# Kernel tuning notes

Measured on AMD Instinct MI355X. Metric: run time of the kernel, lower is better.

## Reference

```python
import jax, jax.numpy as jnp
import numpy as np

EPS = 1e-5

def _bn_relu_over_batch(x, gamma, beta):
    # x: [..., B, F] where batch axis is -2; per-step training-mode BatchNorm1d
    mu = x.mean(axis=-2, keepdims=True)
    var = ((x - mu) ** 2).mean(axis=-2, keepdims=True)  # biased var (torch BN)
    xn = (x - mu) * jax.lax.rsqrt(var + EPS)
    return jax.nn.relu(xn * gamma + beta)

def setup_inputs() -> dict:
    key = jax.random.key(0)
    ks = jax.random.split(key, 8)
    B, T, D_in, E, C, D_out = 8192, 128, 2, 128, 128, 5
    s = 0.1
    return {
        "inputs": jax.random.normal(ks[0], (B, T, D_in), jnp.float32),
        "W_emb": jax.random.normal(ks[1], (E, D_in), jnp.float32) * s,
        "b_emb": jnp.zeros((E,), jnp.float32),
        "g_emb": jnp.ones((E,), jnp.float32),
        "be_emb": jnp.zeros((E,), jnp.float32),
        "W_ih": jax.random.normal(ks[2], (4 * C, E), jnp.float32) * s,
        "W_hh": jax.random.normal(ks[3], (4 * C, C), jnp.float32) * s,
        "b_ih": jnp.zeros((4 * C,), jnp.float32),
        "b_hh": jnp.zeros((4 * C,), jnp.float32),
        "W_out": jax.random.normal(ks[4], (D_out, C), jnp.float32) * s,
        "b_out": jnp.zeros((D_out,), jnp.float32),
        "g_out": jnp.ones((D_out,), jnp.float32),
        "be_out": jnp.zeros((D_out,), jnp.float32),
    }

def reference(inputs, W_emb, b_emb, g_emb, be_emb, W_ih, W_hh, b_ih, b_hh,
              W_out, b_out, g_out, be_out):
    B, T, _ = inputs.shape
    C = W_hh.shape[1]
    # Input embedding: Linear + per-step BatchNorm (batch stats) + ReLU, vectorized over T
    x = jnp.einsum('btd,ed->bte', inputs, W_emb) + b_emb      # [B,T,E]
    x = jnp.transpose(x, (1, 0, 2))                           # [T,B,E]
    x = _bn_relu_over_batch(x, g_emb, be_emb)                 # BN over batch per step

    def step(carry, xt):
        h, c = carry
        gates = xt @ W_ih.T + b_ih + h @ W_hh.T + b_hh        # [B,4C]
        i, f, g, o = jnp.split(gates, 4, axis=-1)             # torch LSTMCell order
        i = jax.nn.sigmoid(i); f = jax.nn.sigmoid(f)
        g = jnp.tanh(g); o = jax.nn.sigmoid(o)
        c = f * c + i * g
        h = o * jnp.tanh(c)
        return (h, c), h

    h0 = jnp.zeros((B, C), inputs.dtype)
    _, h_all = jax.lax.scan(step, (h0, h0), x)                # [T,B,C]

    # Output embedding: Linear + per-step BatchNorm + ReLU
    y = jnp.einsum('tbc,oc->tbo', h_all, W_out) + b_out       # [T,B,5]
    y = _bn_relu_over_batch(y, g_out, be_out)
    return jnp.transpose(y, (1, 0, 2))                        # [B,T,5]
```

## Files before the change

kernel.cpp:

```cpp
#include <hip/hip_runtime.h>

typedef __attribute__((ext_vector_type(8))) short short8;
typedef __attribute__((ext_vector_type(4))) float floatx4;
typedef __attribute__((ext_vector_type(4))) unsigned int uint4v;

#define B_TOT 8192
#define T_STEPS 128
#define E_DIM 128
#define C_DIM 128
#define D_OUT 5
#define BN_EPS 1e-5f

#define LOG2E 1.4426950408889634f
#define TWO_LOG2E 2.8853900817779268f

#define WS_WCAT   0u
#define WS_WOUT   (WS_WCAT + 262144u)
#define WS_A0     (WS_WOUT + 4096u)
#define WS_A1     (WS_A0 + 65536u)
#define WS_CC     (WS_A1 + 65536u)
#define WS_STATS  (WS_CC + 65536u)
#define WS_PART   (WS_STATS + 5120u)
#define WS_Y      (WS_PART + 20480u)

__device__ __forceinline__ float bf2f(unsigned short h){
  return __uint_as_float(((unsigned int)h) << 16);
}
__device__ __forceinline__ unsigned short f2b(float v){
  unsigned int u = __float_as_uint(v);
  u += 0x7FFFu + ((u >> 16) & 1u);
  return (unsigned short)(u >> 16);
}
__device__ __forceinline__ unsigned cvt_pk_bf16(float lo, float hi){
  unsigned r;
  asm("v_cvt_pk_bf16_f32 %0, %1, %2" : "=v"(r) : "v"(lo), "v"(hi));
  return r;
}
__device__ __forceinline__ float ldf(const void* p, int i, int bf){
  return bf ? bf2f(((const unsigned short*)p)[i]) : ((const float*)p)[i];
}
__device__ __forceinline__ int sniff_bf(const void* ones){
  return *(const unsigned int*)ones == 0x3F803F80u;
}

__global__ void k_prep_mom(const void* W_ih, const void* W_hh, const void* W_out,
                           unsigned short* wcat, unsigned short* wout,
                           const void* x, float* part, const void* ones){
  const int bf = sniff_bf(ones);
  const int tid = threadIdx.x;
  if (blockIdx.x < 260){
    int i = blockIdx.x * 512 + tid;
    if (i < 512*256){
      int n = i >> 8, k = i & 255;
      float v = (k < 128) ? ldf(W_ih, n*128 + k, bf) : ldf(W_hh, n*128 + (k-128), bf);
      float sc = ((n >> 7) == 2) ? TWO_LOG2E : -LOG2E;
      wcat[i] = f2b(v * sc);
    } else {
      int j = i - 512*256;
      int n = j >> 7, k = j & 127;
      float v = (n < D_OUT) ? ldf(W_out, n*128 + k, bf) : 0.0f;
      wout[j] = f2b(v);
    }
    return;
  }
  const int mb  = blockIdx.x - 260;
  const int wdw = (mb >> 3) * 8;
  const int rg  = mb & 7;
  const int wv = tid >> 6, lane = tid & 63;
  __shared__ float red[8][16][3];

  if (!bf){
    const float* xp = (const float*)x;
    const int row_b = tid >> 4, j = tid & 15;
    float a0=0, a1=0, a2=0;
    for (int c = 0; c < 32; ++c){
      int row = rg*1024 + c*32 + row_b;
      float v = xp[row*256 + wdw*2 + j];
      float p = __shfl_xor(v, 1, 64);
      if ((j & 1) == 0){ a0 += v; a1 += v*v; a2 += v*p; }
      else             { a0 += v; a1 += v*v; }
    }
    a0 += __shfl_down(a0,32,64); a0 += __shfl_down(a0,16,64);
    a1 += __shfl_down(a1,32,64); a1 += __shfl_down(a1,16,64);
    a2 += __shfl_down(a2,32,64); a2 += __shfl_down(a2,16,64);
    if (lane < 16){ red[wv][lane][0]=a0; red[wv][lane][1]=a1; red[wv][lane][2]=a2; }
  } else {
    const unsigned int* xp = (const unsigned int*)x;
    const int row_b = tid >> 3, j = tid & 7;
    float s0=0,s1=0,s00=0,s11=0,s01=0;
    for (int c = 0; c < 16; ++c){
      int row = rg*1024 + c*64 + row_b;
      unsigned int u = xp[row*128 + wdw + j];
      float xv0 = bf2f((unsigned short)(u & 0xFFFFu));
      float xv1 = bf2f((unsigned short)(u >> 16));
      s0+=xv0; s1+=xv1; s00+=xv0*xv0; s11+=xv1*xv1; s01+=xv0*xv1;
    }
    s0 += __shfl_down(s0,32,64); s0 += __shfl_down(s0,16,64); s0 += __shfl_down(s0,8,64);
    s1 += __shfl_down(s1,32,64); s1 += __shfl_down(s1,16,64); s1 += __shfl_down(s1,8,64);
    s00+= __shfl_down(s00,32,64);s00+= __shfl_down(s00,16,64);s00+= __shfl_down(s00,8,64);
    s11+= __shfl_down(s11,32,64);s11+= __shfl_down(s11,16,64);s11+= __shfl_down(s11,8,64);
    s01+= __shfl_down(s01,32,64);s01+= __shfl_down(s01,16,64);s01+= __shfl_down(s01,8,64);
    if (lane < 8){
      red[wv][lane][0]=s0;  red[wv][lane][1]=s00; red[wv][lane][2]=s01;
      red[wv][8+lane][0]=s1; red[wv][8+lane][1]=s11;
    }
  }
  __syncthreads();
  if (tid < 8){
    int tl = tid;
    float S0=0,S1=0,S00=0,S11=0,S01=0;
    for (int w8 = 0; w8 < 8; ++w8){
      if (!bf){
        S0 += red[w8][2*tl][0];   S00 += red[w8][2*tl][1];   S01 += red[w8][2*tl][2];
        S1 += red[w8][2*tl+1][0]; S11 += red[w8][2*tl+1][1];
      } else {
        S0 += red[w8][tl][0];     S00 += red[w8][tl][1];     S01 += red[w8][tl][2];
        S1 += red[w8][8+tl][0];   S11 += red[w8][8+tl][1];
      }
    }
    float* dst = part + rg*640 + (wdw + tl)*5;
    dst[0]=S0; dst[1]=S1; dst[2]=S00; dst[3]=S11; dst[4]=S01;
  }
}

__global__ void k_coef(const float* part, const void* W_emb, const void* g_emb, const void* be_emb,
                       float* A0, float* A1, float* Cc){
  const int bf = sniff_bf(g_emb);
  int i = blockIdx.x*256 + threadIdx.x;
  int t = i >> 7, e = i & 127;
  float S0=0,S1=0,S00=0,S11=0,S01=0;
  for (int rg = 0; rg < 8; ++rg){
    const float* p = part + rg*640 + t*5;
    S0+=p[0]; S1+=p[1]; S00+=p[2]; S11+=p[3]; S01+=p[4];
  }
  const float inv = 1.0f / (float)B_TOT;
  float mu0 = S0*inv, mu1 = S1*inv;
  float v00 = S00*inv - mu0*mu0, v11 = S11*inv - mu1*mu1, c01 = S01*inv - mu0*mu1;
  float w0 = ldf(W_emb, e*2, bf), w1 = ldf(W_emb, e*2+1, bf);
  float g  = ldf(g_emb, e, bf),  be = ldf(be_emb, e, bf);
  float var = w0*w0*v00 + 2.0f*w0*w1*c01 + w1*w1*v11;
  float rs = rsqrtf(var + BN_EPS);
  float a0 = g*rs*w0, a1 = g*rs*w1;
  A0[i] = a0; A1[i] = a1;
  Cc[i] = be - (a0*mu0 + a1*mu1);
}

__global__ __launch_bounds__(512, 2)
void k_lstm(const void* x, const void* b_ih, const void* b_hh, const void* ones,
            const unsigned short* __restrict__ wcat, const unsigned short* __restrict__ wout,
            const float* __restrict__ A0, const float* __restrict__ A1, const float* __restrict__ Cc,
            float* __restrict__ y_ws){
  const int bf = sniff_bf(ones);
  const int tid = threadIdx.x;
  const int wid = tid >> 6, lane = tid & 63;
  const int q = lane >> 4, s = lane & 15;
  const int row0 = blockIdx.x * 32;

  __shared__ unsigned short xh[2][32][264];

  {
    short8 z;
#pragma unroll
    for (int j = 0; j < 8; ++j) z[j] = 0;
    unsigned short* base = &xh[0][0][0];
    for (int i = tid*8; i < 2*32*264; i += 512*8)
      *(short8*)(base + i) = z;
  }

  short8 bfr[4][8];
#pragma unroll
  for (int gq = 0; gq < 4; ++gq)
#pragma unroll
    for (int ks = 0; ks < 8; ++ks)
      bfr[gq][ks] = *(const short8*)(wcat + ((wid + 8*gq)*16 + s)*256 + ks*32 + q*8);

  short8 wf[4];
#pragma unroll
  for (int ks = 0; ks < 4; ++ks)
    wf[ks] = *(const short8*)(wout + s*128 + ks*32 + q*8);

  const int ch = 16*wid + s;
  floatx4 binit[4];
#pragma unroll
  for (int gq = 0; gq < 4; ++gq){
    float braw = ldf(b_ih, gq*128 + ch, bf) + ldf(b_hh, gq*128 + ch, bf);
    float b = braw * ((gq == 2) ? TWO_LOG2E : -LOG2E);
    binit[gq] = (floatx4){b, b, b, b};
  }

  float c_st[2][4] = {{0,0,0,0},{0,0,0,0}};

  const int r_loc = tid >> 4;
  const int e0 = (tid & 15) * 8;

  auto compute_xe = [&](int tt, int buf){
    float x0, x1;
    int xbase = ((row0 + r_loc)*T_STEPS + tt)*2;
    if (bf){
      unsigned u = ((const unsigned int*)x)[xbase >> 1];
      x0 = __uint_as_float(u << 16);
      x1 = __uint_as_float(u & 0xFFFF0000u);
    } else { const float* xp = (const float*)x; x0 = xp[xbase]; x1 = xp[xbase+1]; }
    floatx4 a0a = *(const floatx4*)(A0 + tt*E_DIM + e0);
    floatx4 a0b = *(const floatx4*)(A0 + tt*E_DIM + e0 + 4);
    floatx4 a1a = *(const floatx4*)(A1 + tt*E_DIM + e0);
    floatx4 a1b = *(const floatx4*)(A1 + tt*E_DIM + e0 + 4);
    floatx4 cca = *(const floatx4*)(Cc + tt*E_DIM + e0);
    floatx4 ccb = *(const floatx4*)(Cc + tt*E_DIM + e0 + 4);
    float v[8];
#pragma unroll
    for (int j = 0; j < 4; ++j){
      v[j]   = fmaxf(fmaf(a0a[j], x0, fmaf(a1a[j], x1, cca[j])), 0.0f);
      v[4+j] = fmaxf(fmaf(a0b[j], x0, fmaf(a1b[j], x1, ccb[j])), 0.0f);
    }
    unsigned w0 = cvt_pk_bf16(v[0], v[1]);
    unsigned w1 = cvt_pk_bf16(v[2], v[3]);
    unsigned w2 = cvt_pk_bf16(v[4], v[5]);
    unsigned w3 = cvt_pk_bf16(v[6], v[7]);
    *(uint4v*)&xh[buf][r_loc][e0] = (uint4v){w0, w1, w2, w3};
  };

  auto cell = [&](const floatx4* acc, float* cs, int mt, int nb){
    float hv[4];
#pragma unroll
    for (int r = 0; r < 4; ++r){
      float ea = __builtin_amdgcn_exp2f(acc[0][r]);
      float eb = __builtin_amdgcn_exp2f(acc[1][r]);
      float ec = __builtin_amdgcn_exp2f(acc[2][r]);
      float ed = __builtin_amdgcn_exp2f(acc[3][r]);
      float Aa = 1.0f + ea, Bb = 1.0f + eb, Ca = 1.0f + ec;
      float t1 = Aa * Ca;
      float r1 = __builtin_amdgcn_rcpf(t1 * Bb);
      float cn = fmaf(t1 * r1, cs[r], (Bb * r1) * (ec - 1.0f));
      cs[r] = cn;
      float E  = __builtin_amdgcn_exp2f(fminf(cn * TWO_LOG2E, 80.0f));
      float r2 = __builtin_amdgcn_rcpf((1.0f + ed) * (E + 1.0f));
      hv[r] = (E - 1.0f) * r2;
    }
    unsigned wlo = cvt_pk_bf16(hv[0], hv[1]);
    unsigned whi = cvt_pk_bf16(hv[2], hv[3]);
    const int rowb = 16*mt + q*4;
    xh[nb][rowb    ][128 + ch] = (unsigned short)(wlo);
    xh[nb][rowb + 1][128 + ch] = (unsigned short)(wlo >> 16);
    xh[nb][rowb + 2][128 + ch] = (unsigned short)(whi);
    xh[nb][rowb + 3][128 + ch] = (unsigned short)(whi >> 16);
  };

  auto step = [&](int t, int cb, int nb){
    if (wid < 2 && t > 0){
      floatx4 ya = {0,0,0,0};
#pragma unroll
      for (int ks = 0; ks < 4; ++ks){
        short8 a = *(const short8*)&xh[cb][s + 16*wid][128 + ks*32 + q*8];
        ya = __builtin_amdgcn_mfma_f32_16x16x32_bf16(a, wf[ks], ya, 0, 0, 0);
      }
      if (s < D_OUT){
#pragma unroll
        for (int r = 0; r < 4; ++r){
          int row = row0 + 16*wid + q*4 + r;
          y_ws[((t-1)*B_TOT + row)*D_OUT + s] = ya[r];
        }
      }
    }

    floatx4 acc0[4], acc1[4];

    {
      short8 a0 = *(const short8*)&xh[cb][s][q*8];
#pragma unroll
      for (int gq = 0; gq < 4; ++gq)
        acc0[gq] = __builtin_amdgcn_mfma_f32_16x16x32_bf16(a0, bfr[gq][0], binit[gq], 0, 0, 0);
    }
#pragma unroll
    for (int ks = 1; ks < 8; ++ks){
      short8 a0 = *(const short8*)&xh[cb][s][ks*32 + q*8];
#pragma unroll
      for (int gq = 0; gq < 4; ++gq)
        acc0[gq] = __builtin_amdgcn_mfma_f32_16x16x32_bf16(a0, bfr[gq][ks], acc0[gq], 0, 0, 0);
    }
    {
      short8 a1 = *(const short8*)&xh[cb][s + 16][q*8];
#pragma unroll
      for (int gq = 0; gq < 4; ++gq)
        acc1[gq] = __builtin_amdgcn_mfma_f32_16x16x32_bf16(a1, bfr[gq][0], binit[gq], 0, 0, 0);
    }
#pragma unroll
    for (int ks = 1; ks < 8; ++ks){
      short8 a1 = *(const short8*)&xh[cb][s + 16][ks*32 + q*8];
#pragma unroll
      for (int gq = 0; gq < 4; ++gq)
        acc1[gq] = __builtin_amdgcn_mfma_f32_16x16x32_bf16(a1, bfr[gq][ks], acc1[gq], 0, 0, 0);
    }

    if (t < T_STEPS-1) compute_xe(t+1, nb);

    cell(acc0, c_st[0], 0, nb);
    cell(acc1, c_st[1], 1, nb);

    __syncthreads();
  };

  __syncthreads();
  compute_xe(0, 0);
  __syncthreads();

  for (int tb = 0; tb < T_STEPS; tb += 2){
    step(tb,     0, 1);
    step(tb + 1, 1, 0);
  }

  if (wid < 2){
    floatx4 ya = {0,0,0,0};
#pragma unroll
    for (int ks = 0; ks < 4; ++ks){
      short8 a = *(const short8*)&xh[0][s + 16*wid][128 + ks*32 + q*8];
      ya = __builtin_amdgcn_mfma_f32_16x16x32_bf16(a, wf[ks], ya, 0, 0, 0);
    }
    if (s < D_OUT){
#pragma unroll
      for (int r = 0; r < 4; ++r){
        int row = row0 + 16*wid + q*4 + r;
        y_ws[((T_STEPS-1)*B_TOT + row)*D_OUT + s] = ya[r];
      }
    }
  }
  asm volatile("s_waitcnt vmcnt(0)" ::: "memory");
}

__global__ void k_outstats(const float* __restrict__ y_ws, const void* g_out, const void* be_out,
                           float* stats, const void* ones){
  const int bf = sniff_bf(ones);
  const int t = blockIdx.x, tid = threadIdx.x;
  __shared__ float acc2[5][2];
  if (tid < 10) ((float*)acc2)[tid] = 0.0f;
  __syncthreads();
  float s[5] = {0,0,0,0,0}, ss[5] = {0,0,0,0,0};
  const floatx4* base = (const floatx4*)(y_ws + (size_t)t * 40960);
#pragma unroll 5
  for (int it = 0; it < 40; ++it){
    floatx4 v = base[it*256 + tid];
#pragma unroll
    for (int j = 0; j < 4; ++j){
      int p = (4*it + j) % 5;
      s[p] += v[j]; ss[p] += v[j]*v[j];
    }
  }
  int ob = (4*tid) % 5;
#pragma unroll
  for (int p = 0; p < 5; ++p){
    int o = ob + p; if (o >= 5) o -= 5;
    atomicAdd(&acc2[o][0], s[p]);
    atomicAdd(&acc2[o][1], ss[p]);
  }
  __syncthreads();
  if (tid < 5){
    float S = acc2[tid][0], SS = acc2[tid][1];
    const float inv = 1.0f / (float)B_TOT;
    float mu = S*inv, var = SS*inv - mu*mu;
    float g = ldf(g_out, tid, bf), be = ldf(be_out, tid, bf);
    float sc = g * rsqrtf(var + BN_EPS);
    stats[(t*5+tid)*2]   = sc;
    stats[(t*5+tid)*2+1] = be - sc*mu;
  }
}

__global__ void k_apply(const float* __restrict__ y_ws, const float* __restrict__ stats,
                        void* out, const void* ones){
  const int bf = sniff_bf(ones);
  __shared__ float tile[128*85];
  const int b0 = blockIdx.x * 16;
  const int tid = threadIdx.x;
  for (int i = tid; i < 10240; i += 256){
    int t = i / 80, j = i - t*80;
    tile[t*85 + j] = y_ws[((size_t)t*B_TOT + b0)*D_OUT + j];
  }
  __syncthreads();
  for (int i = tid; i < 10240; i += 256){
    int b = i / 640, r = i - b*640;
    int t = r / 5, o = r - t*5;
    float v = tile[t*85 + b*5 + o];
    v = fmaxf(fmaf(v, stats[r*2], stats[r*2+1]), 0.0f);
    int oi = b0*640 + i;
    if (bf) ((unsigned short*)out)[oi] = f2b(v);
    else    ((float*)out)[oi] = v;
  }
}

extern "C" void kernel_launch(void* const* d_in, const int* in_sizes, int n_in,
                              void* d_out, int out_size, void* d_ws, size_t ws_size,
                              hipStream_t stream){
  const void* x      = d_in[0];
  const void* W_emb  = d_in[1];
  const void* g_emb  = d_in[3];
  const void* be_emb = d_in[4];
  const void* W_ih   = d_in[5];
  const void* W_hh   = d_in[6];
  const void* b_ih   = d_in[7];
  const void* b_hh   = d_in[8];
  const void* W_out  = d_in[9];
  const void* g_out  = d_in[11];
  const void* be_out = d_in[12];

  char* ws = (char*)d_ws;
  unsigned short* wcat = (unsigned short*)(ws + WS_WCAT);
  unsigned short* wout = (unsigned short*)(ws + WS_WOUT);
  float* A0    = (float*)(ws + WS_A0);
  float* A1    = (float*)(ws + WS_A1);
  float* Cc    = (float*)(ws + WS_CC);
  float* stats = (float*)(ws + WS_STATS);
  float* part  = (float*)(ws + WS_PART);
  float* y_ws  = (float*)(ws + WS_Y);

  k_prep_mom<<<dim3(388),  dim3(512), 0, stream>>>(W_ih, W_hh, W_out, wcat, wout, x, part, g_emb);
  k_coef    <<<dim3(64),   dim3(256), 0, stream>>>(part, W_emb, g_emb, be_emb, A0, A1, Cc);
  k_lstm    <<<dim3(256),  dim3(512), 0, stream>>>(x, b_ih, b_hh, g_emb, wcat, wout, A0, A1, Cc, y_ws);
  k_outstats<<<dim3(128),  dim3(256), 0, stream>>>(y_ws, g_out, be_out, stats, g_emb);
  k_apply   <<<dim3(512),  dim3(256), 0, stream>>>(y_ws, stats, d_out, g_emb);
}
```

Measured before the change: 375.3 us.

## Fuse output BN statistics into LSTM kernel via atomics, drop stats kernel

The LSTM kernel now reduces each step's output-projection sums and sums of squares with wave shuffles and global atomics, so the separate output-statistics kernel and its full pass over y are removed. The y workspace layout changes to [t][o][b], which allows vectorized float4 stores and coalesced reads in the apply kernel. The apply kernel now computes scale and bias from the accumulated sums itself. The cost is extra atomics and shuffle work inside the latency-critical recurrent loop, plus a buffer that must be zeroed by the prep kernel.

```diff
diff --git a/kernel.cpp b/kernel.cpp
--- a/kernel.cpp
+++ b/kernel.cpp
@@ -19,8 +19,8 @@
 #define WS_A0     (WS_WOUT + 4096u)
 #define WS_A1     (WS_A0 + 65536u)
 #define WS_CC     (WS_A1 + 65536u)
-#define WS_STATS  (WS_CC + 65536u)
-#define WS_PART   (WS_STATS + 5120u)
+#define WS_YSUM   (WS_CC + 65536u)
+#define WS_PART   (WS_YSUM + 5120u)
 #define WS_Y      (WS_PART + 20480u)
 
 __device__ __forceinline__ float bf2f(unsigned short h){
@@ -45,9 +45,12 @@
 
 __global__ void k_prep_mom(const void* W_ih, const void* W_hh, const void* W_out,
                            unsigned short* wcat, unsigned short* wout,
-                           const void* x, float* part, const void* ones){
+                           const void* x, float* part, float* ysum, const void* ones){
   const int bf = sniff_bf(ones);
   const int tid = threadIdx.x;
+  if (blockIdx.x == 0){
+    for (int i2 = tid; i2 < 1280; i2 += 512) ysum[i2] = 0.0f;
+  }
   if (blockIdx.x < 260){
     int i = blockIdx.x * 512 + tid;
     if (i < 512*256){
@@ -149,7 +152,7 @@
 void k_lstm(const void* x, const void* b_ih, const void* b_hh, const void* ones,
             const unsigned short* __restrict__ wcat, const unsigned short* __restrict__ wout,
             const float* __restrict__ A0, const float* __restrict__ A1, const float* __restrict__ Cc,
-            float* __restrict__ y_ws){
+            float* __restrict__ y_ws, float* __restrict__ ysum){
   const int bf = sniff_bf(ones);
   const int tid = threadIdx.x;
   const int wid = tid >> 6, lane = tid & 63;
@@ -246,22 +249,27 @@
     xh[nb][rowb + 3][128 + ch] = (unsigned short)(whi >> 16);
   };
 
+  auto do_y = [&](int tt, int hb){
+    floatx4 ya = {0,0,0,0};
+#pragma unroll
+    for (int ks = 0; ks < 4; ++ks){
+      short8 a = *(const short8*)&xh[hb][s + 16*wid][128 + ks*32 + q*8];
+      ya = __builtin_amdgcn_mfma_f32_16x16x32_bf16(a, wf[ks], ya, 0, 0, 0);
+    }
+    if (s < D_OUT)
+      *(floatx4*)(y_ws + ((size_t)tt*D_OUT + s)*B_TOT + row0 + 16*wid + 4*q) = ya;
+    float ps  = ya[0] + ya[1] + ya[2] + ya[3];
+    float pss = ya[0]*ya[0] + ya[1]*ya[1] + ya[2]*ya[2] + ya[3]*ya[3];
+    ps  += __shfl_down(ps, 32, 64); ps  += __shfl_down(ps, 16, 64);
+    pss += __shfl_down(pss, 32, 64); pss += __shfl_down(pss, 16, 64);
+    if (lane < D_OUT){
+      atomicAdd(&ysum[(tt*D_OUT + lane)*2],     ps);
+      atomicAdd(&ysum[(tt*D_OUT + lane)*2 + 1], pss);
+    }
+  };
+
   auto step = [&](int t, int cb, int nb){
-    if (wid < 2 && t > 0){
-      floatx4 ya = {0,0,0,0};
-#pragma unroll
-      for (int ks = 0; ks < 4; ++ks){
-        short8 a = *(const short8*)&xh[cb][s + 16*wid][128 + ks*32 + q*8];
-        ya = __builtin_amdgcn_mfma_f32_16x16x32_bf16(a, wf[ks], ya, 0, 0, 0);
-      }
-      if (s < D_OUT){
-#pragma unroll
-        for (int r = 0; r < 4; ++r){
-          int row = row0 + 16*wid + q*4 + r;
-          y_ws[((t-1)*B_TOT + row)*D_OUT + s] = ya[r];
-        }
-      }
-    }
+    if (wid < 2 && t > 0) do_y(t-1, cb);
 
     floatx4 acc0[4], acc1[4];
 
@@ -309,77 +317,36 @@
     step(tb + 1, 1, 0);
   }
 
-  if (wid < 2){
-    floatx4 ya = {0,0,0,0};
-#pragma unroll
-    for (int ks = 0; ks < 4; ++ks){
-      short8 a = *(const short8*)&xh[0][s + 16*wid][128 + ks*32 + q*8];
-      ya = __builtin_amdgcn_mfma_f32_16x16x32_bf16(a, wf[ks], ya, 0, 0, 0);
-    }
-    if (s < D_OUT){
-#pragma unroll
-      for (int r = 0; r < 4; ++r){
-        int row = row0 + 16*wid + q*4 + r;
-        y_ws[((T_STEPS-1)*B_TOT + row)*D_OUT + s] = ya[r];
-      }
-    }
-  }
+  if (wid < 2) do_y(T_STEPS-1, 0);
+
   asm volatile("s_waitcnt vmcnt(0)" ::: "memory");
 }
 
-__global__ void k_outstats(const float* __restrict__ y_ws, const void* g_out, const void* be_out,
-                           float* stats, const void* ones){
+__global__ void k_apply(const float* __restrict__ y_ws, const float* __restrict__ ysum,
+                        void* out, const void* g_out, const void* be_out, const void* ones){
   const int bf = sniff_bf(ones);
-  const int t = blockIdx.x, tid = threadIdx.x;
-  __shared__ float acc2[5][2];
-  if (tid < 10) ((float*)acc2)[tid] = 0.0f;
-  __syncthreads();
-  float s[5] = {0,0,0,0,0}, ss[5] = {0,0,0,0,0};
-  const floatx4* base = (const floatx4*)(y_ws + (size_t)t * 40960);
-#pragma unroll 5
-  for (int it = 0; it < 40; ++it){
-    floatx4 v = base[it*256 + tid];
-#pragma unroll
-    for (int j = 0; j < 4; ++j){
-      int p = (4*it + j) % 5;
-      s[p] += v[j]; ss[p] += v[j]*v[j];
-    }
-  }
-  int ob = (4*tid) % 5;
-#pragma unroll
-  for (int p = 0; p < 5; ++p){
-    int o = ob + p; if (o >= 5) o -= 5;
-    atomicAdd(&acc2[o][0], s[p]);
-    atomicAdd(&acc2[o][1], ss[p]);
-  }
-  __syncthreads();
-  if (tid < 5){
-    float S = acc2[tid][0], SS = acc2[tid][1];
+  __shared__ float sc_l[640], bi_l[640];
+  __shared__ float tile[10240];
+  const int b0 = blockIdx.x * 16;
+  const int tid = threadIdx.x;
+  for (int i = tid; i < 640; i += 256){
+    float S = ysum[i*2], SS = ysum[i*2+1];
     const float inv = 1.0f / (float)B_TOT;
     float mu = S*inv, var = SS*inv - mu*mu;
-    float g = ldf(g_out, tid, bf), be = ldf(be_out, tid, bf);
+    int o = i % 5;
+    float g = ldf(g_out, o, bf), be = ldf(be_out, o, bf);
     float sc = g * rsqrtf(var + BN_EPS);
-    stats[(t*5+tid)*2]   = sc;
-    stats[(t*5+tid)*2+1] = be - sc*mu;
-  }
-}
-
-__global__ void k_apply(const float* __restrict__ y_ws, const float* __restrict__ stats,
-                        void* out, const void* ones){
-  const int bf = sniff_bf(ones);
-  __shared__ float tile[128*85];
-  const int b0 = blockIdx.x * 16;
-  const int tid = threadIdx.x;
+    sc_l[i] = sc; bi_l[i] = be - sc*mu;
+  }
   for (int i = tid; i < 10240; i += 256){
-    int t = i / 80, j = i - t*80;
-    tile[t*85 + j] = y_ws[((size_t)t*B_TOT + b0)*D_OUT + j];
+    int chunk = i >> 4, j = i & 15;
+    tile[i] = y_ws[(size_t)chunk*B_TOT + b0 + j];
   }
   __syncthreads();
   for (int i = tid; i < 10240; i += 256){
     int b = i / 640, r = i - b*640;
-    int t = r / 5, o = r - t*5;
-    float v = tile[t*85 + b*5 + o];
-    v = fmaxf(fmaf(v, stats[r*2], stats[r*2+1]), 0.0f);
+    float v = tile[r*16 + b];
+    v = fmaxf(fmaf(v, sc_l[r], bi_l[r]), 0.0f);
     int oi = b0*640 + i;
     if (bf) ((unsigned short*)out)[oi] = f2b(v);
     else    ((float*)out)[oi] = v;
@@ -407,13 +374,12 @@
   float* A0    = (float*)(ws + WS_A0);
   float* A1    = (float*)(ws + WS_A1);
   float* Cc    = (float*)(ws + WS_CC);
-  float* stats = (float*)(ws + WS_STATS);
+  float* ysum  = (float*)(ws + WS_YSUM);
   float* part  = (float*)(ws + WS_PART);
   float* y_ws  = (float*)(ws + WS_Y);
 
-  k_prep_mom<<<dim3(388),  dim3(512), 0, stream>>>(W_ih, W_hh, W_out, wcat, wout, x, part, g_emb);
+  k_prep_mom<<<dim3(388),  dim3(512), 0, stream>>>(W_ih, W_hh, W_out, wcat, wout, x, part, ysum, g_emb);
   k_coef    <<<dim3(64),   dim3(256), 0, stream>>>(part, W_emb, g_emb, be_emb, A0, A1, Cc);
-  k_lstm    <<<dim3(256),  dim3(512), 0, stream>>>(x, b_ih, b_hh, g_emb, wcat, wout, A0, A1, Cc, y_ws);
-  k_outstats<<<dim3(128),  dim3(256), 0, stream>>>(y_ws, g_out, be_out, stats, g_emb);
-  k_apply   <<<dim3(512),  dim3(256), 0, stream>>>(y_ws, stats, d_out, g_emb);
-}
+  k_lstm    <<<dim3(256),  dim3(512), 0, stream>>>(x, b_ih, b_hh, g_emb, wcat, wout, A0, A1, Cc, y_ws, ysum);
+  k_apply   <<<dim3(512),  dim3(256), 0, stream>>>(y_ws, ysum, d_out, g_out, be_out, g_emb);
+}
```

After: 463.5 us. +23.5%, slower.
